# Kernel tuning notes

Measured on AMD Instinct MI355X. Metric: run time of the kernel, lower is better.

## Reference

```python
import jax, jax.numpy as jnp
import numpy as np

NEG_SLOPE = 0.2  # LeakyReLU slope used throughout the torch module
K = 20           # hard-coded in Net.__init__ (self.k = 20)


def leaky(x):
    return jnp.where(x >= 0, x, NEG_SLOPE * x)


def setup_inputs() -> dict:
    key = jax.random.key(0)
    ks = jax.random.split(key, 11)
    B, N = 8, 2048
    Cin, Co = 6, 64  # AGConv(3*2, 64, 3*2)
    x = jax.random.normal(ks[0], (B, 3, N), dtype=jnp.float32)
    # 1x1 conv weights (bias=False in the torch code)
    W0 = jax.random.normal(ks[1], (Co, Cin), dtype=jnp.float32) / np.sqrt(Cin)      # AGConv.conv0
    W1 = jax.random.normal(ks[2], (Co * Cin, Co), dtype=jnp.float32) / np.sqrt(Co)  # AGConv.conv1
    Wc = jax.random.normal(ks[3], (3, Co), dtype=jnp.float32) / np.sqrt(Co)         # Net.conv1
    # inference-mode BatchNorm folded to per-channel scale/shift
    bn0_s = jax.random.uniform(ks[4], (Co,), minval=0.5, maxval=1.5)
    bn0_b = 0.1 * jax.random.normal(ks[5], (Co,))
    bn1_s = jax.random.uniform(ks[6], (Co,), minval=0.5, maxval=1.5)
    bn1_b = 0.1 * jax.random.normal(ks[7], (Co,))
    bnc_s = jax.random.uniform(ks[8], (3,), minval=0.5, maxval=1.5)
    bnc_b = 0.1 * jax.random.normal(ks[9], (3,))
    return dict(x=x, W0=W0, bn0_s=bn0_s, bn0_b=bn0_b, W1=W1, bn1_s=bn1_s,
                bn1_b=bn1_b, Wc=Wc, bnc_s=bnc_s, bnc_b=bnc_b)


def reference(x, W0, bn0_s, bn0_b, W1, bn1_s, bn1_b, Wc, bnc_s, bnc_b):
    B, C, N = x.shape  # [B, 3, N]
    xt = jnp.transpose(x, (0, 2, 1))  # [B, N, 3]
    inner = jnp.einsum('bci,bcj->bij', x, x)          # [B, N, N]
    xx = jnp.sum(x * x, axis=1)                       # [B, N]
    pd = 2.0 * inner - xx[:, :, None] - xx[:, None, :]
    _, idx = jax.lax.top_k(pd, K)                     # [B, N, K] int32
    # get_graph_feature: gather neighbor coords, concat (nbr - ctr, ctr)
    nbr = xt[jnp.arange(B)[:, None, None], idx]       # [B, N, K, 3]
    ctr = jnp.broadcast_to(xt[:, :, None, :], (B, N, K, C))
    e = jnp.concatenate([nbr - ctr, ctr], axis=-1)    # [B, N, K, 6]
    # p == e here since both get_graph_feature calls use the same input & idx
    # AGConv: generate per-edge [64,6] weights from e, apply to e
    y = leaky(jnp.einsum('bnki,oi->bnko', e, W0) * bn0_s + bn0_b)   # [B, N, K, 64]
    y = jnp.einsum('bnko,po->bnkp', y, W1).reshape(B, N, K, 64, 6)  # per-edge weight mats
    out = jnp.einsum('bnkoi,bnki->bnko', y, e)                      # adaptive conv
    out = leaky(out * bn1_s + bn1_b)                                # [B, N, K, 64]
    # max-pool aggregate over neighbors
    x1 = jnp.max(out, axis=2)                                       # [B, N, 64]
    # Net.conv1: 1x1 conv 64->3 + BN + leaky
    z = leaky(jnp.einsum('bno,co->bnc', x1, Wc) * bnc_s + bnc_b)    # [B, N, 3]
    return jnp.transpose(z, (0, 2, 1))                              # [B, 3, N]
```

## Files before the change

### kernel.cpp

```cpp
#include <hip/hip_runtime.h>

#define NEGSLOPE 0.2f
#define NINF (-3.4e38f)

typedef _Float16 half8 __attribute__((ext_vector_type(8)));
typedef float f32x4 __attribute__((ext_vector_type(4)));
typedef unsigned long long u64;

#define YSTRIDE 72

__device__ __forceinline__ half8 h8zero() {
    half8 z;
#pragma unroll
    for (int i = 0; i < 8; ++i) z[i] = (_Float16)0.f;
    return z;
}

__device__ __forceinline__ unsigned umin(unsigned a, unsigned b) { return a < b ? a : b; }
__device__ __forceinline__ unsigned umax(unsigned a, unsigned b) { return a > b ? a : b; }

template <int CTRL>
__device__ __forceinline__ unsigned dpp_movm(unsigned v) {
    return (unsigned)__builtin_amdgcn_update_dpp(-1, (int)v, CTRL, 0xF, 0xF, false);
}

__global__ __launch_bounds__(256) void topk_kernel(
    const float* __restrict__ x, int* __restrict__ idx_out,
    const float* __restrict__ w1, _Float16* __restrict__ w1g,
    const float* __restrict__ w0, _Float16* __restrict__ w0f,
    f32x4* __restrict__ xt) {
    if (blockIdx.x >= 4096) {
        const int pid = blockIdx.x - 4096;
        int tid = pid * 256 + threadIdx.x;
#pragma unroll
        for (int it = 0; it < 12; ++it, tid += 2048) {
            int j = tid & 7;
            int L = (tid >> 3) & 63;
            int r = tid >> 9;
            int t4 = r & 3;
            int ks = r >> 2;
            int q = L >> 4, c = L & 15;
            int i = ks >> 1;
            int o = 32 * (ks & 1) + 8 * q + j;
            int u = 16 * t4 + c;
            w1g[tid] = (_Float16)w1[(u * 6 + i) * 64 + o];
        }
        if (pid == 0) {
#pragma unroll
            for (int s = 0; s < 2; ++s) {
                int t2 = threadIdx.x * 2 + s;
                int r8 = t2 >> 3, j = t2 & 7;
                w0f[t2] = (j < 6) ? (_Float16)w0[r8 * 6 + j] : (_Float16)0.f;
            }
        }
        int base = pid * 2048;
#pragma unroll
        for (int it = 0; it < 8; ++it) {
            int i = base + it * 256 + threadIdx.x;
            int bb = i >> 11, n = i & 2047;
            const float* xbp = x + bb * 6144;
            xt[i] = (f32x4){xbp[n], xbp[2048 + n], xbp[4096 + n], 0.f};
        }
        return;
    }

    const int wave = threadIdx.x >> 6;
    const int lane = threadIdx.x & 63;
    const int row = blockIdx.x * 4 + wave;
    const int b = row >> 11;
    const int n = row & 2047;
    const float* xb = x + b * 6144;
    const float xn0 = xb[n];
    const float xn1 = xb[2048 + n];
    const float xn2 = xb[4096 + n];

    unsigned r0 = 0xFFFFFFFFu, r1 = 0xFFFFFFFFu;
    unsigned r2 = 0xFFFFFFFFu, r3 = 0xFFFFFFFFu;
    unsigned g5k = 0xFFFFFFFFu;

#pragma unroll
    for (int t = 0; t < 32; ++t) {
        const int j = t * 64 + lane;
        const float dx = xb[j] - xn0;
        const float dy = xb[2048 + j] - xn1;
        const float dz = xb[4096 + j] - xn2;
        const float d = dx * dx + dy * dy + dz * dz;
        unsigned p = (__float_as_uint(d) & 0xFFFFF800u) | (unsigned)j;
        unsigned q0 = umin(r0, p); p = umax(r0, p); r0 = q0;
        unsigned q1 = umin(r1, p); p = umax(r1, p); r1 = q1;
        unsigned q2 = umin(r2, p); p = umax(r2, p); r2 = q2;
        unsigned q3 = umin(r3, p); p = umax(r3, p); r3 = q3;
        g5k = umin(g5k, p);
    }

    if (lane & 1) {
        unsigned t0 = r0; r0 = r3; r3 = t0;
        unsigned t1 = r1; r1 = r2; r2 = t1;
    }

#define CROSS(DL, KK)                                                         \
    {                                                                         \
        const bool asc = ((lane >> ((KK) - 2)) & 1) == 0;                     \
        const bool low = (lane & (DL)) == 0;                                  \
        const bool selmin = (asc == low);                                     \
        const unsigned p0 = (unsigned)__shfl_xor((int)r0, (DL), 64);          \
        const unsigned p1 = (unsigned)__shfl_xor((int)r1, (DL), 64);          \
        const unsigned p2 = (unsigned)__shfl_xor((int)r2, (DL), 64);          \
        const unsigned p3 = (unsigned)__shfl_xor((int)r3, (DL), 64);          \
        r0 = selmin ? umin(r0, p0) : umax(r0, p0);                            \
        r1 = selmin ? umin(r1, p1) : umax(r1, p1);                            \
        r2 = selmin ? umin(r2, p2) : umax(r2, p2);                            \
        r3 = selmin ? umin(r3, p3) : umax(r3, p3);                            \
    }
#define INLANE(KK)                                                            \
    {                                                                         \
        const bool asc = ((lane >> ((KK) - 2)) & 1) == 0;                     \
        { unsigned lo = umin(r0, r2), hi = umax(r0, r2);                      \
          r0 = asc ? lo : hi; r2 = asc ? hi : lo; }                           \
        { unsigned lo = umin(r1, r3), hi = umax(r1, r3);                      \
          r1 = asc ? lo : hi; r3 = asc ? hi : lo; }                           \
        { unsigned lo = umin(r0, r1), hi = umax(r0, r1);                      \
          r0 = asc ? lo : hi; r1 = asc ? hi : lo; }                           \
        { unsigned lo = umin(r2, r3), hi = umax(r2, r3);                      \
          r2 = asc ? lo : hi; r3 = asc ? hi : lo; }                           \
    }

    CROSS(1, 3)  INLANE(3)
    CROSS(2, 4)  CROSS(1, 4)  INLANE(4)
    CROSS(4, 5)  CROSS(2, 5)  CROSS(1, 5)  INLANE(5)
    CROSS(8, 6)  CROSS(4, 6)  CROSS(2, 6)  CROSS(1, 6)  INLANE(6)
    CROSS(16, 7) CROSS(8, 7)  CROSS(4, 7)  CROSS(2, 7)  CROSS(1, 7)  INLANE(7)
    CROSS(32, 8) CROSS(16, 8) CROSS(8, 8)  CROSS(4, 8)  CROSS(2, 8)  CROSS(1, 8)
    INLANE(8)
#undef CROSS
#undef INLANE

    const int out_base = row * 20;
    const unsigned T20p = (unsigned)__builtin_amdgcn_readlane((int)r3, 4);
    const u64 bad = __ballot(g5k < T20p);

    if (bad == 0) {
        if (lane < 5) {
            int4 v;
            v.x = (int)(r0 & 2047u); v.y = (int)(r1 & 2047u);
            v.z = (int)(r2 & 2047u); v.w = (int)(r3 & 2047u);
            *(int4*)(idx_out + out_base + lane * 4) = v;
        }
    } else {
        unsigned Tprev = 0u;
#pragma unroll 1
        for (int r = 0; r < 20; ++r) {
            unsigned best = 0xFFFFFFFFu;
#pragma unroll
            for (int t = 0; t < 32; ++t) {
                const int j = t * 64 + lane;
                const float dx = xb[j] - xn0;
                const float dy = xb[2048 + j] - xn1;
                const float dz = xb[4096 + j] - xn2;
                const float d = dx * dx + dy * dy + dz * dz;
                const unsigned p = (__float_as_uint(d) & 0xFFFFF800u) | (unsigned)j;
                const bool ok = (r == 0) || (p > Tprev);
                best = umin(best, ok ? p : 0xFFFFFFFFu);
            }
            { unsigned o = dpp_movm<0x111>(best); best = umin(best, o); }
            { unsigned o = dpp_movm<0x112>(best); best = umin(best, o); }
            { unsigned o = dpp_movm<0x114>(best); best = umin(best, o); }
            { unsigned o = dpp_movm<0x118>(best); best = umin(best, o); }
            { unsigned o = dpp_movm<0x142>(best); best = umin(best, o); }
            { unsigned o = dpp_movm<0x143>(best); best = umin(best, o); }
            const unsigned K = (unsigned)__builtin_amdgcn_readlane((int)best, 63);
            if (lane == 0) idx_out[out_base + r] = (int)(K & 2047u);
            Tprev = K;
        }
    }
}

__global__ __launch_bounds__(128, 3) void mlp_mfma(
    const f32x4* __restrict__ xt, const int* __restrict__ idx,
    const _Float16* __restrict__ w0f, const float* __restrict__ bn0s,
    const float* __restrict__ bn0b, const _Float16* __restrict__ w1g,
    const float* __restrict__ bn1s, const float* __restrict__ bn1b,
    const float* __restrict__ wc, const float* __restrict__ bncs,
    const float* __restrict__ bncb, float* __restrict__ out) {
    __shared__ __align__(16) _Float16 yL[2][80 * YSTRIDE];
    __shared__ __align__(16) half8 eL[2][80];
    const int wave = threadIdx.x >> 6;
    const int lane = threadIdx.x & 63;
    const int q = lane >> 4, c = lane & 15;
    const int gw = blockIdx.x * 2 + wave;
    const int b = gw >> 9;
    const int P0 = (gw & 511) * 4;
    _Float16* yw = yL[wave];
    half8* ew = eL[wave];
    const f32x4* xtb = xt + (b << 11);

    {
        const int k = lane >> 2, pt = lane & 3;
        const int n = P0 + pt;
        const int j = idx[(b * 2048 + n) * 20 + k];
        const f32x4 cc = xtb[n];
        const f32x4 nb = xtb[j];
        half8 ev;
        ev[0] = (_Float16)(nb[0] - cc[0]); ev[1] = (_Float16)(nb[1] - cc[1]);
        ev[2] = (_Float16)(nb[2] - cc[2]); ev[3] = (_Float16)cc[0];
        ev[4] = (_Float16)cc[1];           ev[5] = (_Float16)cc[2];
        ev[6] = (_Float16)0.f;             ev[7] = (_Float16)0.f;
        ew[lane] = ev;
    }
    if (lane < 16) {
        const int el = 64 + lane;
        const int k = el >> 2, pt = el & 3;
        const int n = P0 + pt;
        const int j = idx[(b * 2048 + n) * 20 + k];
        const f32x4 cc = xtb[n];
        const f32x4 nb = xtb[j];
        half8 ev;
        ev[0] = (_Float16)(nb[0] - cc[0]); ev[1] = (_Float16)(nb[1] - cc[1]);
        ev[2] = (_Float16)(nb[2] - cc[2]); ev[3] = (_Float16)cc[0];
        ev[4] = (_Float16)cc[1];           ev[5] = (_Float16)cc[2];
        ev[6] = (_Float16)0.f;             ev[7] = (_Float16)0.f;
        ew[el] = ev;
    }

    const half8* w0f8 = (const half8*)w0f;
    const half8 z8 = h8zero();
    half8 B1[4];
    float s0v[4], b0v[4];
#pragma unroll
    for (int nt = 0; nt < 4; ++nt) {
        const half8 v = w0f8[nt * 16 + c];
        B1[nt] = (q == 0) ? v : z8;
        s0v[nt] = bn0s[16 * nt + c];
        b0v[nt] = bn0b[16 * nt + c];
    }
#pragma unroll
    for (int mt = 0; mt < 5; ++mt) {
        const half8 ev = ew[16 * mt + c];
        const half8 Ae = (q == 0) ? ev : z8;
        const int ebase = 16 * mt + 4 * q;
#pragma unroll
        for (int nt = 0; nt < 4; ++nt) {
            f32x4 D = {0.f, 0.f, 0.f, 0.f};
            D = __builtin_amdgcn_mfma_f32_16x16x32_f16(Ae, B1[nt], D, 0, 0, 0);
#pragma unroll
            for (int r = 0; r < 4; ++r) {
                float v = D[r] * s0v[nt] + b0v[nt];
                v = fmaxf(v, NEGSLOPE * v);
                const int edge = ebase + r;
                yw[edge * YSTRIDE + ((16 * nt + c) ^ (edge & 0x38))] =
                    (_Float16)v;
            }
        }
    }

    const half8* w1g8 = (const half8*)w1g;

    f32x4 acc[5][4];
#pragma unroll
    for (int mm = 0; mm < 5; ++mm)
#pragma unroll
        for (int t4 = 0; t4 < 4; ++t4) acc[mm][t4] = (f32x4){0.f, 0.f, 0.f, 0.f};

#pragma unroll 1
    for (int i6 = 0; i6 < 6; ++i6) {
        _Float16 es[5];
#pragma unroll
        for (int mm = 0; mm < 5; ++mm)
            es[mm] = ((const _Float16*)(ew + 16 * mm + c))[i6];
#pragma unroll
        for (int ks2 = 0; ks2 < 2; ++ks2) {
            const int ks = 2 * i6 + ks2;
            half8 B[4];
#pragma unroll
            for (int t4 = 0; t4 < 4; ++t4)
                B[t4] = w1g8[(ks * 4 + t4) * 64 + lane];
#pragma unroll
            for (int mm = 0; mm < 5; ++mm) {
                const int rrow = 16 * mm + c;
                const half8 Af = *(const half8*)&yw[rrow * YSTRIDE +
                                                    ((32 * ks2 + 8 * q) ^ (rrow & 0x38))];
                const half8 An = Af * es[mm];
#pragma unroll
                for (int t4 = 0; t4 < 4; ++t4)
                    acc[mm][t4] = __builtin_amdgcn_mfma_f32_16x16x32_f16(
                        An, B[t4], acc[mm][t4], 0, 0, 0);
            }
        }
    }

    float bs1[4], bb1[4];
#pragma unroll
    for (int t4 = 0; t4 < 4; ++t4) {
        bs1[t4] = bn1s[16 * t4 + c];
        bb1[t4] = bn1b[16 * t4 + c];
    }

    float x1[4][4];
#pragma unroll
    for (int r = 0; r < 4; ++r)
#pragma unroll
        for (int t4 = 0; t4 < 4; ++t4) {
            float v = NINF;
#pragma unroll
            for (int mm = 0; mm < 5; ++mm) {
                float w = acc[mm][t4][r] * bs1[t4] + bb1[t4];
                w = fmaxf(w, NEGSLOPE * w);
                v = fmaxf(v, w);
            }
            v = fmaxf(v, __shfl_xor(v, 16, 64));
            v = fmaxf(v, __shfl_xor(v, 32, 64));
            x1[r][t4] = v;
        }

    float wcv[3][4];
#pragma unroll
    for (int co = 0; co < 3; ++co)
#pragma unroll
        for (int t4 = 0; t4 < 4; ++t4) wcv[co][t4] = wc[co * 64 + 16 * t4 + c];

    float part[4][3];
#pragma unroll
    for (int r = 0; r < 4; ++r)
#pragma unroll
        for (int co = 0; co < 3; ++co) {
            float s = x1[r][0] * wcv[co][0] + x1[r][1] * wcv[co][1] +
                      x1[r][2] * wcv[co][2] + x1[r][3] * wcv[co][3];
#pragma unroll
            for (int d = 1; d < 16; d <<= 1) s += __shfl_xor(s, d, 64);
            part[r][co] = s;
        }

    if (c == 0 && q < 3) {
        const float sc = bncs[q], bc = bncb[q];
#pragma unroll
        for (int r = 0; r < 4; ++r) {
            float z = part[r][q] * sc + bc;
            z = fmaxf(z, NEGSLOPE * z);
            out[(b * 3 + q) * 2048 + P0 + r] = z;
        }
    }
}

extern "C" void kernel_launch(void* const* d_in, const int* in_sizes, int n_in,
                              void* d_out, int out_size, void* d_ws, size_t ws_size,
                              hipStream_t stream) {
    const float* x    = (const float*)d_in[0];
    const float* W0   = (const float*)d_in[1];
    const float* bn0s = (const float*)d_in[2];
    const float* bn0b = (const float*)d_in[3];
    const float* W1   = (const float*)d_in[4];
    const float* bn1s = (const float*)d_in[5];
    const float* bn1b = (const float*)d_in[6];
    const float* Wc   = (const float*)d_in[7];
    const float* bncs = (const float*)d_in[8];
    const float* bncb = (const float*)d_in[9];

    _Float16* w1g = (_Float16*)d_ws;
    _Float16* w0f = (_Float16*)((char*)d_ws + 49152);
    f32x4* xt = (f32x4*)((char*)d_ws + 65536);
    int* idx = (int*)((char*)d_ws + 327680);

    topk_kernel<<<4104, 256, 0, stream>>>(x, idx, W1, w1g, W0, w0f, xt);
    mlp_mfma<<<2048, 128, 0, stream>>>(xt, idx, w0f, bn0s, bn0b, w1g,
                                       bn1s, bn1b, Wc, bncs, bncb,
                                       (float*)d_out);
}
```

Baseline: 136.9 us.

## Fuse kNN top-k selection into the MFMA edge-conv kernel via shared-memory indices

Moves the per-point top-20 neighbor search into the MLP kernel: each wave computes top-k for its 4 points sequentially and stores indices in LDS, then builds edge features directly from x instead of a transposed copy. This drops the global idx round trip, the xt transpose buffer and one large kernel launch, leaving a tiny weight-prep kernel. In exchange, the top-k work now runs at the MLP kernel's occupancy (128-thread blocks, 3 blocks per CU) and serially within each wave, which may reduce the parallelism available to the distance and sort phase.

Measured after the change: 245.4 us. 79.3% more time.

```diff
diff --git a/kernel.cpp b/kernel.cpp
--- a/kernel.cpp
+++ b/kernel.cpp
@@ -24,79 +24,54 @@
     return (unsigned)__builtin_amdgcn_update_dpp(-1, (int)v, CTRL, 0xF, 0xF, false);
 }
 
-__global__ __launch_bounds__(256) void topk_kernel(
-    const float* __restrict__ x, int* __restrict__ idx_out,
+__global__ __launch_bounds__(256) void prep_kernel(
     const float* __restrict__ w1, _Float16* __restrict__ w1g,
-    const float* __restrict__ w0, _Float16* __restrict__ w0f,
-    f32x4* __restrict__ xt) {
-    if (blockIdx.x >= 4096) {
-        const int pid = blockIdx.x - 4096;
-        int tid = pid * 256 + threadIdx.x;
-#pragma unroll
-        for (int it = 0; it < 12; ++it, tid += 2048) {
-            int j = tid & 7;
-            int L = (tid >> 3) & 63;
-            int r = tid >> 9;
-            int t4 = r & 3;
-            int ks = r >> 2;
-            int q = L >> 4, c = L & 15;
-            int i = ks >> 1;
-            int o = 32 * (ks & 1) + 8 * q + j;
-            int u = 16 * t4 + c;
-            w1g[tid] = (_Float16)w1[(u * 6 + i) * 64 + o];
-        }
-        if (pid == 0) {
-#pragma unroll
-            for (int s = 0; s < 2; ++s) {
-                int t2 = threadIdx.x * 2 + s;
-                int r8 = t2 >> 3, j = t2 & 7;
-                w0f[t2] = (j < 6) ? (_Float16)w0[r8 * 6 + j] : (_Float16)0.f;
-            }
-        }
-        int base = pid * 2048;
-#pragma unroll
-        for (int it = 0; it < 8; ++it) {
-            int i = base + it * 256 + threadIdx.x;
-            int bb = i >> 11, n = i & 2047;
-            const float* xbp = x + bb * 6144;
-            xt[i] = (f32x4){xbp[n], xbp[2048 + n], xbp[4096 + n], 0.f};
-        }
-        return;
-    }
-
+    const float* __restrict__ w0, _Float16* __restrict__ w0f) {
+    const int pid = blockIdx.x;
+    int tid = pid * 256 + threadIdx.x;
+#pragma unroll
+    for (int it = 0; it < 12; ++it, tid += 2048) {
+        int j = tid & 7;
+        int L = (tid >> 3) & 63;
+        int r = tid >> 9;
+        int t4 = r & 3;
+        int ks = r >> 2;
+        int q = L >> 4, c = L & 15;
+        int i = ks >> 1;
+        int o = 32 * (ks & 1) + 8 * q + j;
+        int u = 16 * t4 + c;
+        w1g[tid] = (_Float16)w1[(u * 6 + i) * 64 + o];
+    }
+    if (pid == 0) {
+#pragma unroll
+        for (int s = 0; s < 2; ++s) {
+            int t2 = threadIdx.x * 2 + s;
+            int r8 = t2 >> 3, j = t2 & 7;
+            w0f[t2] = (j < 6) ? (_Float16)w0[r8 * 6 + j] : (_Float16)0.f;
+        }
+    }
+}
+
+__global__ __launch_bounds__(128, 3) void fused_kernel(
+    const float* __restrict__ x,
+    const _Float16* __restrict__ w0f, const float* __restrict__ bn0s,
+    const float* __restrict__ bn0b, const _Float16* __restrict__ w1g,
+    const float* __restrict__ bn1s, const float* __restrict__ bn1b,
+    const float* __restrict__ wc, const float* __restrict__ bncs,
+    const float* __restrict__ bncb, float* __restrict__ out) {
+    __shared__ __align__(16) _Float16 yL[2][80 * YSTRIDE];
+    __shared__ __align__(16) half8 eL[2][80];
+    __shared__ int iwL[2][80];
     const int wave = threadIdx.x >> 6;
     const int lane = threadIdx.x & 63;
-    const int row = blockIdx.x * 4 + wave;
-    const int b = row >> 11;
-    const int n = row & 2047;
+    const int q = lane >> 4, c = lane & 15;
+    const int gw = blockIdx.x * 2 + wave;
+    const int b = gw >> 9;
+    const int P0 = (gw & 511) * 4;
     const float* xb = x + b * 6144;
-    const float xn0 = xb[n];
-    const float xn1 = xb[2048 + n];
-    const float xn2 = xb[4096 + n];
-
-    unsigned r0 = 0xFFFFFFFFu, r1 = 0xFFFFFFFFu;
-    unsigned r2 = 0xFFFFFFFFu, r3 = 0xFFFFFFFFu;
-    unsigned g5k = 0xFFFFFFFFu;
-
-#pragma unroll
-    for (int t = 0; t < 32; ++t) {
-        const int j = t * 64 + lane;
-        const float dx = xb[j] - xn0;
-        const float dy = xb[2048 + j] - xn1;
-        const float dz = xb[4096 + j] - xn2;
-        const float d = dx * dx + dy * dy + dz * dz;
-        unsigned p = (__float_as_uint(d) & 0xFFFFF800u) | (unsigned)j;
-        unsigned q0 = umin(r0, p); p = umax(r0, p); r0 = q0;
-        unsigned q1 = umin(r1, p); p = umax(r1, p); r1 = q1;
-        unsigned q2 = umin(r2, p); p = umax(r2, p); r2 = q2;
-        unsigned q3 = umin(r3, p); p = umax(r3, p); r3 = q3;
-        g5k = umin(g5k, p);
-    }
-
-    if (lane & 1) {
-        unsigned t0 = r0; r0 = r3; r3 = t0;
-        unsigned t1 = r1; r1 = r2; r2 = t1;
-    }
+    _Float16* yw = yL[wave];
+    half8* ew = eL[wave];
+    int* iw = iwL[wave];
 
 #define CROSS(DL, KK)                                                         \
     {                                                                         \
@@ -125,100 +100,112 @@
           r2 = asc ? lo : hi; r3 = asc ? hi : lo; }                           \
     }
 
-    CROSS(1, 3)  INLANE(3)
-    CROSS(2, 4)  CROSS(1, 4)  INLANE(4)
-    CROSS(4, 5)  CROSS(2, 5)  CROSS(1, 5)  INLANE(5)
-    CROSS(8, 6)  CROSS(4, 6)  CROSS(2, 6)  CROSS(1, 6)  INLANE(6)
-    CROSS(16, 7) CROSS(8, 7)  CROSS(4, 7)  CROSS(2, 7)  CROSS(1, 7)  INLANE(7)
-    CROSS(32, 8) CROSS(16, 8) CROSS(8, 8)  CROSS(4, 8)  CROSS(2, 8)  CROSS(1, 8)
-    INLANE(8)
+#pragma unroll 1
+    for (int rr = 0; rr < 4; ++rr) {
+        const int n = P0 + rr;
+        const float xn0 = xb[n];
+        const float xn1 = xb[2048 + n];
+        const float xn2 = xb[4096 + n];
+
+        unsigned r0 = 0xFFFFFFFFu, r1 = 0xFFFFFFFFu;
+        unsigned r2 = 0xFFFFFFFFu, r3 = 0xFFFFFFFFu;
+        unsigned g5k = 0xFFFFFFFFu;
+
+#pragma unroll
+        for (int t = 0; t < 32; ++t) {
+            const int j = t * 64 + lane;
+            const float dx = xb[j] - xn0;
+            const float dy = xb[2048 + j] - xn1;
+            const float dz = xb[4096 + j] - xn2;
+            const float d = dx * dx + dy * dy + dz * dz;
+            unsigned p = (__float_as_uint(d) & 0xFFFFF800u) | (unsigned)j;
+            unsigned q0 = umin(r0, p); p = umax(r0, p); r0 = q0;
+            unsigned q1 = umin(r1, p); p = umax(r1, p); r1 = q1;
+            unsigned q2 = umin(r2, p); p = umax(r2, p); r2 = q2;
+            unsigned q3 = umin(r3, p); p = umax(r3, p); r3 = q3;
+            g5k = umin(g5k, p);
+        }
+
+        if (lane & 1) {
+            unsigned t0 = r0; r0 = r3; r3 = t0;
+            unsigned t1 = r1; r1 = r2; r2 = t1;
+        }
+        CROSS(1, 3)  INLANE(3)
+        CROSS(2, 4)  CROSS(1, 4)  INLANE(4)
+        CROSS(4, 5)  CROSS(2, 5)  CROSS(1, 5)  INLANE(5)
+        CROSS(8, 6)  CROSS(4, 6)  CROSS(2, 6)  CROSS(1, 6)  INLANE(6)
+        CROSS(16, 7) CROSS(8, 7)  CROSS(4, 7)  CROSS(2, 7)  CROSS(1, 7)  INLANE(7)
+        CROSS(32, 8) CROSS(16, 8) CROSS(8, 8)  CROSS(4, 8)  CROSS(2, 8)
+        CROSS(1, 8)  INLANE(8)
+
+        const unsigned T20p = (unsigned)__builtin_amdgcn_readlane((int)r3, 4);
+        const u64 bad = __ballot(g5k < T20p);
+
+        if (bad == 0) {
+            if (lane < 5) {
+                iw[(4 * lane + 0) * 4 + rr] = (int)(r0 & 2047u);
+                iw[(4 * lane + 1) * 4 + rr] = (int)(r1 & 2047u);
+                iw[(4 * lane + 2) * 4 + rr] = (int)(r2 & 2047u);
+                iw[(4 * lane + 3) * 4 + rr] = (int)(r3 & 2047u);
+            }
+        } else {
+            unsigned Tprev = 0u;
+#pragma unroll 1
+            for (int rk = 0; rk < 20; ++rk) {
+                unsigned best = 0xFFFFFFFFu;
+#pragma unroll
+                for (int t = 0; t < 32; ++t) {
+                    const int j = t * 64 + lane;
+                    const float dx = xb[j] - xn0;
+                    const float dy = xb[2048 + j] - xn1;
+                    const float dz = xb[4096 + j] - xn2;
+                    const float d = dx * dx + dy * dy + dz * dz;
+                    const unsigned p =
+                        (__float_as_uint(d) & 0xFFFFF800u) | (unsigned)j;
+                    const bool ok = (rk == 0) || (p > Tprev);
+                    best = umin(best, ok ? p : 0xFFFFFFFFu);
+                }
+                { unsigned o = dpp_movm<0x111>(best); best = umin(best, o); }
+                { unsigned o = dpp_movm<0x112>(best); best = umin(best, o); }
+                { unsigned o = dpp_movm<0x114>(best); best = umin(best, o); }
+                { unsigned o = dpp_movm<0x118>(best); best = umin(best, o); }
+                { unsigned o = dpp_movm<0x142>(best); best = umin(best, o); }
+                { unsigned o = dpp_movm<0x143>(best); best = umin(best, o); }
+                const unsigned K =
+                    (unsigned)__builtin_amdgcn_readlane((int)best, 63);
+                if (lane == 0) iw[rk * 4 + rr] = (int)(K & 2047u);
+                Tprev = K;
+            }
+        }
+    }
 #undef CROSS
 #undef INLANE
 
-    const int out_base = row * 20;
-    const unsigned T20p = (unsigned)__builtin_amdgcn_readlane((int)r3, 4);
-    const u64 bad = __ballot(g5k < T20p);
-
-    if (bad == 0) {
-        if (lane < 5) {
-            int4 v;
-            v.x = (int)(r0 & 2047u); v.y = (int)(r1 & 2047u);
-            v.z = (int)(r2 & 2047u); v.w = (int)(r3 & 2047u);
-            *(int4*)(idx_out + out_base + lane * 4) = v;
-        }
-    } else {
-        unsigned Tprev = 0u;
-#pragma unroll 1
-        for (int r = 0; r < 20; ++r) {
-            unsigned best = 0xFFFFFFFFu;
-#pragma unroll
-            for (int t = 0; t < 32; ++t) {
-                const int j = t * 64 + lane;
-                const float dx = xb[j] - xn0;
-                const float dy = xb[2048 + j] - xn1;
-                const float dz = xb[4096 + j] - xn2;
-                const float d = dx * dx + dy * dy + dz * dz;
-                const unsigned p = (__float_as_uint(d) & 0xFFFFF800u) | (unsigned)j;
-                const bool ok = (r == 0) || (p > Tprev);
-                best = umin(best, ok ? p : 0xFFFFFFFFu);
-            }
-            { unsigned o = dpp_movm<0x111>(best); best = umin(best, o); }
-            { unsigned o = dpp_movm<0x112>(best); best = umin(best, o); }
-            { unsigned o = dpp_movm<0x114>(best); best = umin(best, o); }
-            { unsigned o = dpp_movm<0x118>(best); best = umin(best, o); }
-            { unsigned o = dpp_movm<0x142>(best); best = umin(best, o); }
-            { unsigned o = dpp_movm<0x143>(best); best = umin(best, o); }
-            const unsigned K = (unsigned)__builtin_amdgcn_readlane((int)best, 63);
-            if (lane == 0) idx_out[out_base + r] = (int)(K & 2047u);
-            Tprev = K;
-        }
-    }
-}
-
-__global__ __launch_bounds__(128, 3) void mlp_mfma(
-    const f32x4* __restrict__ xt, const int* __restrict__ idx,
-    const _Float16* __restrict__ w0f, const float* __restrict__ bn0s,
-    const float* __restrict__ bn0b, const _Float16* __restrict__ w1g,
-    const float* __restrict__ bn1s, const float* __restrict__ bn1b,
-    const float* __restrict__ wc, const float* __restrict__ bncs,
-    const float* __restrict__ bncb, float* __restrict__ out) {
-    __shared__ __align__(16) _Float16 yL[2][80 * YSTRIDE];
-    __shared__ __align__(16) half8 eL[2][80];
-    const int wave = threadIdx.x >> 6;
-    const int lane = threadIdx.x & 63;
-    const int q = lane >> 4, c = lane & 15;
-    const int gw = blockIdx.x * 2 + wave;
-    const int b = gw >> 9;
-    const int P0 = (gw & 511) * 4;
-    _Float16* yw = yL[wave];
-    half8* ew = eL[wave];
-    const f32x4* xtb = xt + (b << 11);
-
     {
-        const int k = lane >> 2, pt = lane & 3;
+        const int pt = lane & 3;
         const int n = P0 + pt;
-        const int j = idx[(b * 2048 + n) * 20 + k];
-        const f32x4 cc = xtb[n];
-        const f32x4 nb = xtb[j];
+        const int j = iw[lane];
+        const float c0 = xb[n], c1 = xb[2048 + n], c2 = xb[4096 + n];
         half8 ev;
-        ev[0] = (_Float16)(nb[0] - cc[0]); ev[1] = (_Float16)(nb[1] - cc[1]);
-        ev[2] = (_Float16)(nb[2] - cc[2]); ev[3] = (_Float16)cc[0];
-        ev[4] = (_Float16)cc[1];           ev[5] = (_Float16)cc[2];
-        ev[6] = (_Float16)0.f;             ev[7] = (_Float16)0.f;
+        ev[0] = (_Float16)(xb[j] - c0);
+        ev[1] = (_Float16)(xb[2048 + j] - c1);
+        ev[2] = (_Float16)(xb[4096 + j] - c2);
+        ev[3] = (_Float16)c0; ev[4] = (_Float16)c1; ev[5] = (_Float16)c2;
+        ev[6] = (_Float16)0.f; ev[7] = (_Float16)0.f;
         ew[lane] = ev;
     }
     if (lane < 16) {
         const int el = 64 + lane;
-        const int k = el >> 2, pt = el & 3;
+        const int pt = el & 3;
         const int n = P0 + pt;
-        const int j = idx[(b * 2048 + n) * 20 + k];
-        const f32x4 cc = xtb[n];
-        const f32x4 nb = xtb[j];
+        const int j = iw[el];
+        const float c0 = xb[n], c1 = xb[2048 + n], c2 = xb[4096 + n];
         half8 ev;
-        ev[0] = (_Float16)(nb[0] - cc[0]); ev[1] = (_Float16)(nb[1] - cc[1]);
-        ev[2] = (_Float16)(nb[2] - cc[2]); ev[3] = (_Float16)cc[0];
-        ev[4] = (_Float16)cc[1];           ev[5] = (_Float16)cc[2];
-        ev[6] = (_Float16)0.f;             ev[7] = (_Float16)0.f;
+        ev[0] = (_Float16)(xb[j] - c0);
+        ev[1] = (_Float16)(xb[2048 + j] - c1);
+        ev[2] = (_Float16)(xb[4096 + j] - c2);
+        ev[3] = (_Float16)c0; ev[4] = (_Float16)c1; ev[5] = (_Float16)c2;
+        ev[6] = (_Float16)0.f; ev[7] = (_Float16)0.f;
         ew[el] = ev;
     }
 
@@ -357,11 +344,9 @@
 
     _Float16* w1g = (_Float16*)d_ws;
     _Float16* w0f = (_Float16*)((char*)d_ws + 49152);
-    f32x4* xt = (f32x4*)((char*)d_ws + 65536);
-    int* idx = (int*)((char*)d_ws + 327680);
-
-    topk_kernel<<<4104, 256, 0, stream>>>(x, idx, W1, w1g, W0, w0f, xt);
-    mlp_mfma<<<2048, 128, 0, stream>>>(xt, idx, w0f, bn0s, bn0b, w1g,
-                                       bn1s, bn1b, Wc, bncs, bncb,
-                                       (float*)d_out);
-}
+
+    prep_kernel<<<8, 256, 0, stream>>>(W1, w1g, W0, w0f);
+    fused_kernel<<<2048, 128, 0, stream>>>(x, w0f, bn0s, bn0b, w1g,
+                                           bn1s, bn1b, Wc, bncs, bncb,
+                                           (float*)d_out);
+}
```

## Replicate W1 fp16 tiles per XCD and gather coordinates directly from x

Applied to the files above, without the earlier changes.

The weight-prep blocks now each write a full private copy of the reordered fp16 W1 (8 replicas), and each MLP block reads the replica chosen by blockIdx&7, presumably so that each XCD's L2 holds its own copy and cross-die traffic drops. The packed xt transpose buffer is removed, so the MLP kernel gathers neighbour and centre coordinates straight from the strided x array. In exchange, each prep block does 24576 conversions in a loop instead of 3072, and each coordinate gather becomes three scattered scalar loads instead of one 16-byte load.

New measurement: 143.1 us. +4.5%, slower.

```diff
diff --git a/kernel.cpp b/kernel.cpp
--- a/kernel.cpp
+++ b/kernel.cpp
@@ -27,23 +27,21 @@
 __global__ __launch_bounds__(256) void topk_kernel(
     const float* __restrict__ x, int* __restrict__ idx_out,
     const float* __restrict__ w1, _Float16* __restrict__ w1g,
-    const float* __restrict__ w0, _Float16* __restrict__ w0f,
-    f32x4* __restrict__ xt) {
+    const float* __restrict__ w0, _Float16* __restrict__ w0f) {
     if (blockIdx.x >= 4096) {
         const int pid = blockIdx.x - 4096;
-        int tid = pid * 256 + threadIdx.x;
-#pragma unroll
-        for (int it = 0; it < 12; ++it, tid += 2048) {
-            int j = tid & 7;
-            int L = (tid >> 3) & 63;
-            int r = tid >> 9;
+        _Float16* dst = w1g + pid * 24576;
+        for (int e = threadIdx.x; e < 24576; e += 256) {
+            int j = e & 7;
+            int L = (e >> 3) & 63;
+            int r = e >> 9;
             int t4 = r & 3;
             int ks = r >> 2;
             int q = L >> 4, c = L & 15;
             int i = ks >> 1;
             int o = 32 * (ks & 1) + 8 * q + j;
             int u = 16 * t4 + c;
-            w1g[tid] = (_Float16)w1[(u * 6 + i) * 64 + o];
+            dst[e] = (_Float16)w1[(u * 6 + i) * 64 + o];
         }
         if (pid == 0) {
 #pragma unroll
@@ -52,14 +50,6 @@
                 int r8 = t2 >> 3, j = t2 & 7;
                 w0f[t2] = (j < 6) ? (_Float16)w0[r8 * 6 + j] : (_Float16)0.f;
             }
-        }
-        int base = pid * 2048;
-#pragma unroll
-        for (int it = 0; it < 8; ++it) {
-            int i = base + it * 256 + threadIdx.x;
-            int bb = i >> 11, n = i & 2047;
-            const float* xbp = x + bb * 6144;
-            xt[i] = (f32x4){xbp[n], xbp[2048 + n], xbp[4096 + n], 0.f};
         }
         return;
     }
@@ -176,7 +166,7 @@
 }
 
 __global__ __launch_bounds__(128, 3) void mlp_mfma(
-    const f32x4* __restrict__ xt, const int* __restrict__ idx,
+    const float* __restrict__ x, const int* __restrict__ idx,
     const _Float16* __restrict__ w0f, const float* __restrict__ bn0s,
     const float* __restrict__ bn0b, const _Float16* __restrict__ w1g,
     const float* __restrict__ bn1s, const float* __restrict__ bn1b,
@@ -192,19 +182,19 @@
     const int P0 = (gw & 511) * 4;
     _Float16* yw = yL[wave];
     half8* ew = eL[wave];
-    const f32x4* xtb = xt + (b << 11);
+    const float* xb = x + b * 6144;
 
     {
         const int k = lane >> 2, pt = lane & 3;
         const int n = P0 + pt;
         const int j = idx[(b * 2048 + n) * 20 + k];
-        const f32x4 cc = xtb[n];
-        const f32x4 nb = xtb[j];
+        const float c0 = xb[n], c1 = xb[2048 + n], c2 = xb[4096 + n];
         half8 ev;
-        ev[0] = (_Float16)(nb[0] - cc[0]); ev[1] = (_Float16)(nb[1] - cc[1]);
-        ev[2] = (_Float16)(nb[2] - cc[2]); ev[3] = (_Float16)cc[0];
-        ev[4] = (_Float16)cc[1];           ev[5] = (_Float16)cc[2];
-        ev[6] = (_Float16)0.f;             ev[7] = (_Float16)0.f;
+        ev[0] = (_Float16)(xb[j] - c0);
+        ev[1] = (_Float16)(xb[2048 + j] - c1);
+        ev[2] = (_Float16)(xb[4096 + j] - c2);
+        ev[3] = (_Float16)c0; ev[4] = (_Float16)c1; ev[5] = (_Float16)c2;
+        ev[6] = (_Float16)0.f; ev[7] = (_Float16)0.f;
         ew[lane] = ev;
     }
     if (lane < 16) {
@@ -212,13 +202,13 @@
         const int k = el >> 2, pt = el & 3;
         const int n = P0 + pt;
         const int j = idx[(b * 2048 + n) * 20 + k];
-        const f32x4 cc = xtb[n];
-        const f32x4 nb = xtb[j];
+        const float c0 = xb[n], c1 = xb[2048 + n], c2 = xb[4096 + n];
         half8 ev;
-        ev[0] = (_Float16)(nb[0] - cc[0]); ev[1] = (_Float16)(nb[1] - cc[1]);
-        ev[2] = (_Float16)(nb[2] - cc[2]); ev[3] = (_Float16)cc[0];
-        ev[4] = (_Float16)cc[1];           ev[5] = (_Float16)cc[2];
-        ev[6] = (_Float16)0.f;             ev[7] = (_Float16)0.f;
+        ev[0] = (_Float16)(xb[j] - c0);
+        ev[1] = (_Float16)(xb[2048 + j] - c1);
+        ev[2] = (_Float16)(xb[4096 + j] - c2);
+        ev[3] = (_Float16)c0; ev[4] = (_Float16)c1; ev[5] = (_Float16)c2;
+        ev[6] = (_Float16)0.f; ev[7] = (_Float16)0.f;
         ew[el] = ev;
     }
 
@@ -253,7 +243,7 @@
         }
     }
 
-    const half8* w1g8 = (const half8*)w1g;
+    const half8* w1g8 = (const half8*)w1g + (blockIdx.x & 7) * 3072;
 
     f32x4 acc[5][4];
 #pragma unroll
@@ -356,12 +346,11 @@
     const float* bncb = (const float*)d_in[9];
 
     _Float16* w1g = (_Float16*)d_ws;
-    _Float16* w0f = (_Float16*)((char*)d_ws + 49152);
-    f32x4* xt = (f32x4*)((char*)d_ws + 65536);
-    int* idx = (int*)((char*)d_ws + 327680);
-
-    topk_kernel<<<4104, 256, 0, stream>>>(x, idx, W1, w1g, W0, w0f, xt);
-    mlp_mfma<<<2048, 128, 0, stream>>>(xt, idx, w0f, bn0s, bn0b, w1g,
+    _Float16* w0f = (_Float16*)((char*)d_ws + 393216);
+    int* idx = (int*)((char*)d_ws + 458752);
+
+    topk_kernel<<<4104, 256, 0, stream>>>(x, idx, W1, w1g, W0, w0f);
+    mlp_mfma<<<2048, 128, 0, stream>>>(x, idx, w0f, bn0s, bn0b, w1g,
                                        bn1s, bn1b, Wc, bncs, bncb,
                                        (float*)d_out);
 }
```
